# Optimization experiments

Measured on AMD Instinct MI355X. Metric: run time of the kernel, lower is better.

The kernel has to match this reference:

```python
import jax, jax.numpy as jnp
import numpy as np

B, S, E = 4, 1024, 1024
H, DH = 16, 64
P = 64  # prompt length
MASKED_BIAS = -10000.0


def setup_inputs() -> dict:
    key = jax.random.key(0)
    ks = jax.random.split(key, 9)
    return {
        "hidden_states": jax.random.normal(ks[0], (B, S, E), jnp.float32),
        "promptKey": jax.random.normal(ks[1], (B, H, P, DH), jnp.float32),
        "promptValue": jax.random.normal(ks[2], (B, H, P, DH), jnp.float32),
        "textualKey": jax.random.normal(ks[3], (B, H, S, DH), jnp.float32),
        "textualValue": jax.random.normal(ks[4], (B, H, S, DH), jnp.float32),
        "promptMask": jnp.ones((B, 1, S, P), jnp.bool_),
        "c_attn_w": jax.random.normal(ks[5], (E, 3 * E), jnp.float32) * 0.02,
        "c_attn_b": jnp.zeros((3 * E,), jnp.float32),
        "c_proj_w": jax.random.normal(ks[6], (E, E), jnp.float32) * 0.02,
        "c_proj_b": jnp.zeros((E,), jnp.float32),
    }


def _split_heads(t):
    # [B, S, E] -> [B, H, S, DH]
    b, s, _ = t.shape
    return t.reshape(b, s, H, DH).transpose(0, 2, 1, 3)


def reference(hidden_states, promptKey, promptValue, textualKey, textualValue,
              promptMask, c_attn_w, c_attn_b, c_proj_w, c_proj_b):
    qkv = hidden_states @ c_attn_w + c_attn_b          # [B,S,3E]
    q, k, v = jnp.split(qkv, 3, axis=-1)
    q, k, v = _split_heads(q), _split_heads(k), _split_heads(v)  # [B,H,S,DH]

    # scores against prompt KV, textual KV, and elementwise self term
    promptW = jnp.einsum("bhsd,bhpd->bhsp", q, promptKey)       # [B,H,S,P]
    textW = jnp.einsum("bhsd,bhtd->bhst", q, textualKey)        # [B,H,S,S]
    selfW = jnp.sum(q * k, axis=-1, keepdims=True)              # [B,H,S,1]
    attn_weights = jnp.concatenate((promptW, textW, selfW), axis=-1)
    attn_weights = attn_weights / jnp.sqrt(jnp.float32(DH))

    # non-residual causal mask: bias[qlen-qlen:qlen, 1:klen+1] -> strictly lower tri
    causal = jnp.tri(S, S, -1, dtype=bool)                      # [S,S]
    self_mask = jnp.ones((S, 1), dtype=bool)
    causal_self = jnp.concatenate((causal, self_mask), axis=-1)[None, None]  # [1,1,S,S+1]
    full_mask = jnp.concatenate(
        (promptMask, jnp.broadcast_to(causal_self, (B, 1, S, S + 1))), axis=-1)
    attn_weights = jnp.where(full_mask, attn_weights, MASKED_BIAS)
    attn_weights = jax.nn.softmax(attn_weights, axis=-1)

    wSelf = attn_weights[..., -1:]                              # [B,H,S,1]
    wRest = attn_weights[..., :-1]                              # [B,H,S,P+S]
    valuePast = jnp.concatenate((promptValue, textualValue), axis=-2)  # [B,H,P+S,DH]
    attn_output = jnp.einsum("bhsk,bhkd->bhsd", wRest, valuePast) + wSelf * v

    # merge heads and output projection
    attn_output = attn_output.transpose(0, 2, 1, 3).reshape(B, S, E)
    return attn_output @ c_proj_w + c_proj_b
```

## Files before the change

### kernel.cpp

```cpp
#include <hip/hip_runtime.h>
#include <hip/hip_bf16.h>
#include <stdint.h>

#define H_ 16
#define DH_ 64
#define S_ 1024
#define B_ 4
#define E_ 1024
#define P_ 64
#define BH_ (B_ * H_)
#define KV_ (P_ + S_)
#define NT_ 17
#define TILE_ELEMS 4096

typedef __attribute__((ext_vector_type(8))) short short8;
typedef __attribute__((ext_vector_type(4))) float floatx4;

#define MFMA_BF16(a, b, c) __builtin_amdgcn_mfma_f32_16x16x32_bf16((a), (b), (c), 0, 0, 0)

__device__ __forceinline__ float bf2f(unsigned short u) {
    union { float f; uint32_t i; } x;
    x.i = ((uint32_t)u) << 16;
    return x.f;
}
__device__ __forceinline__ unsigned short f2bf(float f) {
    uint32_t i = __float_as_uint(f);
    uint32_t r = (i + 0x7fffu + ((i >> 16) & 1u)) >> 16;
    return (unsigned short)r;
}

__device__ __forceinline__ void gl_lds16(const void* g, void* l) {
    __builtin_amdgcn_global_load_lds(
        (const __attribute__((address_space(1))) uint32_t*)g,
        (__attribute__((address_space(3))) uint32_t*)l, 16, 0, 0);
}

#define BARRIER() asm volatile("s_barrier" ::: "memory")
#define WAIT_VM(n) asm volatile("s_waitcnt vmcnt(" #n ")" ::: "memory")

__global__ void prep(const float* __restrict__ hidden, const float* __restrict__ cw,
                     const float* __restrict__ pw, const float* __restrict__ pK,
                     const float* __restrict__ tK, const float* __restrict__ pV,
                     const float* __restrict__ tV, unsigned short* __restrict__ Ah,
                     unsigned short* __restrict__ Wt1, unsigned short* __restrict__ Wt2,
                     unsigned short* __restrict__ Kp, unsigned short* __restrict__ Vp) {
    __shared__ float t[32][33];
    int bid = blockIdx.x, tid = threadIdx.x;
    if (bid < 4096) {
        int i = bid * 256 + tid;
        float4 v = ((const float4*)hidden)[i];
        ushort4 o;
        o.x = f2bf(v.x); o.y = f2bf(v.y); o.z = f2bf(v.z); o.w = f2bf(v.w);
        ((ushort4*)Ah)[i] = o;
    } else if (bid < 8192) {
        const float* in; unsigned short* out; int R, C, bxx, byy;
        if (bid < 7168) { int i = bid - 4096; in = cw; out = Wt1; R = 1024; C = 3072; bxx = i % 96; byy = i / 96; }
        else            { int i = bid - 7168; in = pw; out = Wt2; R = 1024; C = 1024; bxx = i % 32; byy = i / 32; }
        int tx = tid & 31, ty = tid >> 5;
        int c0 = bxx * 32, r0 = byy * 32;
#pragma unroll
        for (int i = 0; i < 4; ++i)
            t[ty + i * 8][tx] = in[(size_t)(r0 + ty + i * 8) * C + c0 + tx];
        __syncthreads();
#pragma unroll
        for (int i = 0; i < 4; ++i)
            out[(size_t)(c0 + ty + i * 8) * R + r0 + tx] = f2bf(t[tx][ty + i * 8]);
    } else {
        int gid0 = (bid - 8192) * 256 + tid;
        int half = gid0 / (BH_ * 8704);
        int gid = gid0 % (BH_ * 8704);
        int bh = gid / 8704, rem = gid % 8704;
        int tt = rem / 512, r2 = rem % 512;
        int f = r2 >> 6, lane = r2 & 63;
        int nt = f >> 1, h = f & 1, quad = lane >> 4, cl = lane & 15;
        unsigned short o[8];
        if (half == 0) {
            int key = tt * 64 + nt * 16 + cl;
            int dh = h * 32 + quad * 8;
            const float* src = (key < P_)
                ? pK + ((size_t)bh * P_ + key) * DH_ + dh
                : tK + ((size_t)bh * S_ + (key - P_)) * DH_ + dh;
#pragma unroll
            for (int u = 0; u < 8; ++u) o[u] = f2bf(src[u]);
            *(int4*)&Kp[(size_t)gid * 8] = *(int4*)o;
        } else {
            int dhn = nt * 16 + cl;
            int kbase = tt * 64 + h * 32 + quad * 8;
            const float* src = (kbase < P_)
                ? pV + ((size_t)bh * P_ + kbase) * DH_ + dhn
                : tV + ((size_t)bh * S_ + (kbase - P_)) * DH_ + dhn;
#pragma unroll
            for (int u = 0; u < 8; ++u) o[u] = f2bf(src[(size_t)u * DH_]);
            *(int4*)&Vp[(size_t)gid * 8] = *(int4*)o;
        }
    }
}

template <int MODE, int TM, int TN, int BK>
__global__ __launch_bounds__(256) void gemm_bt(
    const unsigned short* __restrict__ A, const unsigned short* __restrict__ Bt,
    const float* __restrict__ bias, float* __restrict__ Cout,
    unsigned short* __restrict__ Qo, unsigned short* __restrict__ Ko,
    unsigned short* __restrict__ Vo, int M, int N, int K) {
    constexpr int MI = TM / 32, NI = TN / 32;
    constexpr int NA = TM * BK / 2048;
    constexpr int NB = TN * BK / 2048;
    static_assert(NA + NB == 4, "vmcnt constant assumes 4 loads/tile");
    __shared__ __align__(16) unsigned short lA[2][TM * BK];
    __shared__ __align__(16) unsigned short lB[2][TN * BK];
    int tid = threadIdx.x;
    int wave = tid >> 6, lane = tid & 63, quad = lane >> 4, cl = lane & 15;
    int m0 = blockIdx.y * TM, n0 = blockIdx.x * TN;
    int wm = (wave >> 1) * (TM / 2), wn = (wave & 1) * (TN / 2);
    floatx4 acc[MI][NI];
#pragma unroll
    for (int mi = 0; mi < MI; ++mi)
#pragma unroll
        for (int ni = 0; ni < NI; ++ni) acc[mi][ni] = (floatx4){0.f, 0.f, 0.f, 0.f};

    auto issue = [&](int k0, int buf) {
#pragma unroll
        for (int li = 0; li < NA; ++li) {
            int o = (li * 256 + tid) * 16;
            int hh = o / (TM * 64), rr = (o % (TM * 64)) >> 6, c8 = (o >> 4) & 3;
            gl_lds16(A + (size_t)(m0 + rr) * K + k0 + hh * 32 + c8 * 8,
                     (char*)lA[buf] + o);
        }
#pragma unroll
        for (int li = 0; li < NB; ++li) {
            int o = (li * 256 + tid) * 16;
            int hh = o / (TN * 64), rr = (o % (TN * 64)) >> 6, c8 = (o >> 4) & 3;
            gl_lds16(Bt + (size_t)(n0 + rr) * K + k0 + hh * 32 + c8 * 8,
                     (char*)lB[buf] + o);
        }
    };
    auto compute = [&](int buf) {
#pragma unroll
        for (int kk = 0; kk < BK / 32; ++kk) {
            short8 af[MI], bfr[NI];
#pragma unroll
            for (int mi = 0; mi < MI; ++mi)
                af[mi] = *(const short8*)&lA[buf][kk * TM * 32 + (wm + mi * 16 + cl) * 32 + quad * 8];
#pragma unroll
            for (int ni = 0; ni < NI; ++ni)
                bfr[ni] = *(const short8*)&lB[buf][kk * TN * 32 + (wn + ni * 16 + cl) * 32 + quad * 8];
#pragma unroll
            for (int mi = 0; mi < MI; ++mi)
#pragma unroll
                for (int ni = 0; ni < NI; ++ni)
                    acc[mi][ni] = MFMA_BF16(af[mi], bfr[ni], acc[mi][ni]);
        }
    };

    int nT = K / BK;
    issue(0, 0);
    for (int t = 0; t < nT; ++t) {
        int buf = t & 1;
        if (t + 1 < nT) {
            issue((t + 1) * BK, buf ^ 1);
            WAIT_VM(4);
        } else {
            WAIT_VM(0);
        }
        BARRIER();
        compute(buf);
        BARRIER();
    }

#pragma unroll
    for (int ni = 0; ni < NI; ++ni) {
        int ncol = n0 + wn + ni * 16 + cl;
        float bv = bias[ncol];
#pragma unroll
        for (int mi = 0; mi < MI; ++mi) {
#pragma unroll
            for (int r = 0; r < 4; ++r) {
                int mrow = m0 + wm + mi * 16 + quad * 4 + r;
                float v = acc[mi][ni][r] + bv;
                if (MODE == 0) {
                    Cout[(size_t)mrow * N + ncol] = v;
                } else {
                    int which = ncol >> 10, e = ncol & 1023;
                    int hh = e >> 6, dh = e & 63;
                    int b = mrow >> 10, s = mrow & 1023;
                    size_t idx = ((size_t)(b * H_ + hh) * S_ + s) * DH_ + dh;
                    unsigned short* dst = (which == 0) ? Qo : ((which == 1) ? Ko : Vo);
                    dst[idx] = f2bf(v);
                }
            }
        }
    }
}

__global__ __launch_bounds__(256) void attn_k(
    const unsigned short* __restrict__ Q, const unsigned short* __restrict__ Kc,
    const unsigned short* __restrict__ Vc, const unsigned short* __restrict__ Kp,
    const unsigned short* __restrict__ Vp, unsigned short* __restrict__ Aout) {
    __shared__ __align__(16) unsigned short lP[4][16 * 72];
    int tid = threadIdx.x, wave = tid >> 6, lane = tid & 63;
    int quad = lane >> 4, cl = lane & 15;
    int l = blockIdx.x;
    int p = l >> 6, bh = l & 63;
    int b = bh >> 4, h = bh & 15;
    const unsigned short* Qb = Q + (size_t)bh * S_ * DH_;
    const unsigned short* Kb = Kc + (size_t)bh * S_ * DH_;
    const unsigned short* Vb = Vc + (size_t)bh * S_ * DH_;
    const unsigned short* Kpb = Kp + (size_t)bh * NT_ * TILE_ELEMS;
    const unsigned short* Vpb = Vp + (size_t)bh * NT_ * TILE_ELEMS;
    unsigned short* lp = lP[wave];

    int x1 = p, x2 = 15 - p;
    int qb1 = x1 * 64 + wave * 16, qb2 = x2 * 64 + wave * 16;

    short8 a0_1 = *(const short8*)(Qb + (size_t)(qb1 + cl) * DH_ + quad * 8);
    short8 a1_1 = *(const short8*)(Qb + (size_t)(qb1 + cl) * DH_ + quad * 8 + 32);
    short8 a0_2 = *(const short8*)(Qb + (size_t)(qb2 + cl) * DH_ + quad * 8);
    short8 a1_2 = *(const short8*)(Qb + (size_t)(qb2 + cl) * DH_ + quad * 8 + 32);

    float lsum1[4] = {0.f, 0.f, 0.f, 0.f}, lsum2[4] = {0.f, 0.f, 0.f, 0.f};
    floatx4 O1[4], O2[4];
#pragma unroll
    for (int nt = 0; nt < 4; ++nt) {
        O1[nt] = (floatx4){0.f, 0.f, 0.f, 0.f};
        O2[nt] = (floatx4){0.f, 0.f, 0.f, 0.f};
    }

    int rl = wave * 16 + quad * 4;

    auto do_tile = [&](const unsigned short* Kt, const unsigned short* Vt,
                       short8 a0, short8 a1, floatx4* O, float* lsum, bool diag) {
        floatx4 s[4];
        short8 k0[4], k1[4], v0[4], v1[4];
#pragma unroll
        for (int nt = 0; nt < 4; ++nt) {
            k0[nt] = *(const short8*)&Kt[(nt * 2 + 0) * 512 + lane * 8];
            k1[nt] = *(const short8*)&Kt[(nt * 2 + 1) * 512 + lane * 8];
        }
#pragma unroll
        for (int nt = 0; nt < 4; ++nt) {
            s[nt] = (floatx4){0.f, 0.f, 0.f, 0.f};
            s[nt] = MFMA_BF16(a0, k0[nt], s[nt]);
            s[nt] = MFMA_BF16(a1, k1[nt], s[nt]);
        }
#pragma unroll
        for (int nt = 0; nt < 4; ++nt) {
            v0[nt] = *(const short8*)&Vt[(nt * 2 + 0) * 512 + lane * 8];
            v1[nt] = *(const short8*)&Vt[(nt * 2 + 1) * 512 + lane * 8];
        }
#pragma unroll
        for (int nt = 0; nt < 4; ++nt) {
            int col = nt * 16 + cl;
#pragma unroll
            for (int r = 0; r < 4; ++r) {
                float v = s[nt][r] * 0.125f;
                if (diag && col >= rl + r) v = -10000.0f;
                float pb = __expf(v);
                lsum[r] += pb;
                lp[(quad * 4 + r) * 72 + col] = f2bf(pb);
            }
        }
        asm volatile("s_waitcnt lgkmcnt(0)" ::: "memory");
        short8 p0 = *(const short8*)&lp[cl * 72 + quad * 8];
        short8 p1 = *(const short8*)&lp[cl * 72 + quad * 8 + 32];
#pragma unroll
        for (int nt = 0; nt < 4; ++nt) {
            O[nt] = MFMA_BF16(p0, v0[nt], O[nt]);
            O[nt] = MFMA_BF16(p1, v1[nt], O[nt]);
        }
    };

    int T1 = x1 + 2, Tu = x2 + 2;
    for (int t = 0; t < Tu; ++t) {
        const unsigned short* Kt = Kpb + (size_t)t * TILE_ELEMS;
        const unsigned short* Vt = Vpb + (size_t)t * TILE_ELEMS;
        do_tile(Kt, Vt, a0_2, a1_2, O2, lsum2, t == Tu - 1);
        if (t < T1) do_tile(Kt, Vt, a0_1, a1_1, O1, lsum1, t == T1 - 1);
    }

#pragma unroll
    for (int seg = 0; seg < 2; ++seg) {
        int qb = seg ? qb2 : qb1;
        float* lsum = seg ? lsum2 : lsum1;
        floatx4* O = seg ? O2 : O1;
#pragma unroll
        for (int r = 0; r < 4; ++r) {
            float rs = lsum[r];
            rs += __shfl_xor(rs, 1, 16);
            rs += __shfl_xor(rs, 2, 16);
            rs += __shfl_xor(rs, 4, 16);
            rs += __shfl_xor(rs, 8, 16);
            int row = qb + quad * 4 + r;
            const unsigned short* qp = Qb + (size_t)row * DH_ + cl * 4;
            const unsigned short* kp = Kb + (size_t)row * DH_ + cl * 4;
            float d = 0.f;
#pragma unroll
            for (int u = 0; u < 4; ++u) d += bf2f(qp[u]) * bf2f(kp[u]);
            d += __shfl_xor(d, 1, 16);
            d += __shfl_xor(d, 2, 16);
            d += __shfl_xor(d, 4, 16);
            d += __shfl_xor(d, 8, 16);
            float ps = __expf(d * 0.125f);
            float linv = 1.0f / (rs + ps);
#pragma unroll
            for (int nt = 0; nt < 4; ++nt) {
                float vv = bf2f(Vb[(size_t)row * DH_ + nt * 16 + cl]);
                float o = (O[nt][r] + ps * vv) * linv;
                Aout[((size_t)b * S_ + row) * E_ + h * DH_ + nt * 16 + cl] = f2bf(o);
            }
        }
    }
}

extern "C" void kernel_launch(void* const* d_in, const int* in_sizes, int n_in,
                              void* d_out, int out_size, void* d_ws, size_t ws_size,
                              hipStream_t stream) {
    const float* hidden = (const float*)d_in[0];
    const float* pK = (const float*)d_in[1];
    const float* pV = (const float*)d_in[2];
    const float* tK = (const float*)d_in[3];
    const float* tV = (const float*)d_in[4];
    const float* cw = (const float*)d_in[6];
    const float* cb = (const float*)d_in[7];
    const float* pw = (const float*)d_in[8];
    const float* pb = (const float*)d_in[9];
    float* out = (float*)d_out;

    unsigned short* ws = (unsigned short*)d_ws;
    unsigned short* Wt1 = ws;
    unsigned short* Wt2 = Wt1 + (size_t)3072 * 1024;
    unsigned short* Ah  = Wt2 + (size_t)1024 * 1024;
    unsigned short* Qw  = Ah + (size_t)4096 * 1024;
    unsigned short* Kw  = Qw + (size_t)BH_ * S_ * DH_;
    unsigned short* Vw  = Kw + (size_t)BH_ * S_ * DH_;
    unsigned short* Kp  = Vw + (size_t)BH_ * S_ * DH_;
    unsigned short* Vp  = Kp + (size_t)BH_ * NT_ * TILE_ELEMS;
    unsigned short* At  = Ah;

    prep<<<12544, 256, 0, stream>>>(hidden, cw, pw, pK, tK, pV, tV,
                                    Ah, Wt1, Wt2, Kp, Vp);
    gemm_bt<1, 128, 128, 32><<<dim3(3072 / 128, 4096 / 128), 256, 0, stream>>>(
        Ah, Wt1, cb, nullptr, Qw, Kw, Vw, 4096, 3072, 1024);
    attn_k<<<512, 256, 0, stream>>>(Qw, Kw, Vw, Kp, Vp, At);
    gemm_bt<0, 64, 64, 64><<<dim3(1024 / 64, 4096 / 128 * 2), 256, 0, stream>>>(
        At, Wt2, pb, out, nullptr, nullptr, nullptr, 4096, 1024, 1024);
}
```

Before: 200.9 us.

## Add direct-B-load QKV GEMM and split attention into one tile per block

Adds a new QKV projection GEMM that stages only A through LDS with double-buffered async loads and reads the B operand directly from global memory into registers, removing the LDS traffic for B. The attention kernel no longer pairs a short and a long causal query block per workgroup. Each block now handles one 64-row query block, the grid doubles to 1024, and blocks are ordered longest-first for load balance. This trades the explicit balancing of paired work and shared K/V tile loads for more parallelism and fewer live registers per block.

```diff
diff --git a/kernel.cpp b/kernel.cpp
--- a/kernel.cpp
+++ b/kernel.cpp
@@ -192,6 +192,102 @@
     }
 }
 
+__global__ __launch_bounds__(256) void gemm_bd(
+    const unsigned short* __restrict__ A, const unsigned short* __restrict__ Bt,
+    const float* __restrict__ bias, unsigned short* __restrict__ Qo,
+    unsigned short* __restrict__ Ko, unsigned short* __restrict__ Vo,
+    int M, int N, int K) {
+    __shared__ __align__(16) unsigned short lA[2][128 * 32];
+    int tid = threadIdx.x;
+    int wave = tid >> 6, lane = tid & 63, quad = lane >> 4, cl = lane & 15;
+    int m0 = blockIdx.y * 128, n0 = blockIdx.x * 128;
+    int wm = (wave >> 1) * 64, wn = (wave & 1) * 64;
+    floatx4 acc[4][4];
+#pragma unroll
+    for (int mi = 0; mi < 4; ++mi)
+#pragma unroll
+        for (int ni = 0; ni < 4; ++ni) acc[mi][ni] = (floatx4){0.f, 0.f, 0.f, 0.f};
+
+    auto issueA = [&](int k0, int buf) {
+#pragma unroll
+        for (int li = 0; li < 2; ++li) {
+            int o = (li * 256 + tid) * 16;
+            int rr = o >> 6, c8 = (o >> 4) & 3;
+            gl_lds16(A + (size_t)(m0 + rr) * K + k0 + c8 * 8,
+                     (char*)lA[buf] + o);
+        }
+    };
+    const unsigned short* Bbase = Bt + (size_t)(n0 + wn + cl) * K + quad * 8;
+    auto loadB = [&](int k0, short8* dst) {
+#pragma unroll
+        for (int ni = 0; ni < 4; ++ni)
+            dst[ni] = *(const short8*)(Bbase + (size_t)(ni * 16) * K + k0);
+    };
+    auto compute = [&](int buf, const short8* bfr) {
+        short8 af[4];
+#pragma unroll
+        for (int mi = 0; mi < 4; ++mi)
+            af[mi] = *(const short8*)&lA[buf][(wm + mi * 16 + cl) * 32 + quad * 8];
+#pragma unroll
+        for (int mi = 0; mi < 4; ++mi)
+#pragma unroll
+            for (int ni = 0; ni < 4; ++ni)
+                acc[mi][ni] = MFMA_BF16(af[mi], bfr[ni], acc[mi][ni]);
+    };
+
+    int nT = K / 32;
+    short8 bA[4], bB[4];
+    issueA(0, 0);
+    loadB(0, bA);
+    for (int t2 = 0; t2 < nT; t2 += 2) {
+        {
+            int t = t2, buf = t & 1;
+            if (t + 1 < nT) {
+                issueA((t + 1) * 32, buf ^ 1);
+                loadB((t + 1) * 32, bB);
+                WAIT_VM(6);
+            } else {
+                WAIT_VM(0);
+            }
+            BARRIER();
+            compute(buf, bA);
+            BARRIER();
+        }
+        {
+            int t = t2 + 1, buf = t & 1;
+            if (t + 1 < nT) {
+                issueA((t + 1) * 32, buf ^ 1);
+                loadB((t + 1) * 32, bA);
+                WAIT_VM(6);
+            } else {
+                WAIT_VM(0);
+            }
+            BARRIER();
+            compute(buf, bB);
+            BARRIER();
+        }
+    }
+
+#pragma unroll
+    for (int ni = 0; ni < 4; ++ni) {
+        int ncol = n0 + wn + ni * 16 + cl;
+        float bv = bias[ncol];
+        int which = ncol >> 10, e = ncol & 1023;
+        int hh = e >> 6, dh = e & 63;
+        unsigned short* dst = (which == 0) ? Qo : ((which == 1) ? Ko : Vo);
+#pragma unroll
+        for (int mi = 0; mi < 4; ++mi) {
+#pragma unroll
+            for (int r = 0; r < 4; ++r) {
+                int mrow = m0 + wm + mi * 16 + quad * 4 + r;
+                int b = mrow >> 10, s = mrow & 1023;
+                dst[((size_t)(b * H_ + hh) * S_ + s) * DH_ + dh] =
+                    f2bf(acc[mi][ni][r] + bv);
+            }
+        }
+    }
+}
+
 __global__ __launch_bounds__(256) void attn_k(
     const unsigned short* __restrict__ Q, const unsigned short* __restrict__ Kc,
     const unsigned short* __restrict__ Vc, const unsigned short* __restrict__ Kp,
@@ -200,7 +296,7 @@
     int tid = threadIdx.x, wave = tid >> 6, lane = tid & 63;
     int quad = lane >> 4, cl = lane & 15;
     int l = blockIdx.x;
-    int p = l >> 6, bh = l & 63;
+    int x = 15 - (l >> 6), bh = l & 63;
     int b = bh >> 4, h = bh & 15;
     const unsigned short* Qb = Q + (size_t)bh * S_ * DH_;
     const unsigned short* Kb = Kc + (size_t)bh * S_ * DH_;
@@ -209,26 +305,22 @@
     const unsigned short* Vpb = Vp + (size_t)bh * NT_ * TILE_ELEMS;
     unsigned short* lp = lP[wave];
 
-    int x1 = p, x2 = 15 - p;
-    int qb1 = x1 * 64 + wave * 16, qb2 = x2 * 64 + wave * 16;
-
-    short8 a0_1 = *(const short8*)(Qb + (size_t)(qb1 + cl) * DH_ + quad * 8);
-    short8 a1_1 = *(const short8*)(Qb + (size_t)(qb1 + cl) * DH_ + quad * 8 + 32);
-    short8 a0_2 = *(const short8*)(Qb + (size_t)(qb2 + cl) * DH_ + quad * 8);
-    short8 a1_2 = *(const short8*)(Qb + (size_t)(qb2 + cl) * DH_ + quad * 8 + 32);
-
-    float lsum1[4] = {0.f, 0.f, 0.f, 0.f}, lsum2[4] = {0.f, 0.f, 0.f, 0.f};
-    floatx4 O1[4], O2[4];
-#pragma unroll
-    for (int nt = 0; nt < 4; ++nt) {
-        O1[nt] = (floatx4){0.f, 0.f, 0.f, 0.f};
-        O2[nt] = (floatx4){0.f, 0.f, 0.f, 0.f};
-    }
+    int qb = x * 64 + wave * 16;
+
+    short8 a0 = *(const short8*)(Qb + (size_t)(qb + cl) * DH_ + quad * 8);
+    short8 a1 = *(const short8*)(Qb + (size_t)(qb + cl) * DH_ + quad * 8 + 32);
+
+    float lsum[4] = {0.f, 0.f, 0.f, 0.f};
+    floatx4 O[4];
+#pragma unroll
+    for (int nt = 0; nt < 4; ++nt) O[nt] = (floatx4){0.f, 0.f, 0.f, 0.f};
 
     int rl = wave * 16 + quad * 4;
 
-    auto do_tile = [&](const unsigned short* Kt, const unsigned short* Vt,
-                       short8 a0, short8 a1, floatx4* O, float* lsum, bool diag) {
+    int T = x + 2;
+    for (int t = 0; t < T; ++t) {
+        const unsigned short* Kt = Kpb + (size_t)t * TILE_ELEMS;
+        const unsigned short* Vt = Vpb + (size_t)t * TILE_ELEMS;
         floatx4 s[4];
         short8 k0[4], k1[4], v0[4], v1[4];
 #pragma unroll
@@ -247,6 +339,7 @@
             v0[nt] = *(const short8*)&Vt[(nt * 2 + 0) * 512 + lane * 8];
             v1[nt] = *(const short8*)&Vt[(nt * 2 + 1) * 512 + lane * 8];
         }
+        bool diag = (t == T - 1);
 #pragma unroll
         for (int nt = 0; nt < 4; ++nt) {
             int col = nt * 16 + cl;
@@ -267,46 +360,32 @@
             O[nt] = MFMA_BF16(p0, v0[nt], O[nt]);
             O[nt] = MFMA_BF16(p1, v1[nt], O[nt]);
         }
-    };
-
-    int T1 = x1 + 2, Tu = x2 + 2;
-    for (int t = 0; t < Tu; ++t) {
-        const unsigned short* Kt = Kpb + (size_t)t * TILE_ELEMS;
-        const unsigned short* Vt = Vpb + (size_t)t * TILE_ELEMS;
-        do_tile(Kt, Vt, a0_2, a1_2, O2, lsum2, t == Tu - 1);
-        if (t < T1) do_tile(Kt, Vt, a0_1, a1_1, O1, lsum1, t == T1 - 1);
-    }
-
-#pragma unroll
-    for (int seg = 0; seg < 2; ++seg) {
-        int qb = seg ? qb2 : qb1;
-        float* lsum = seg ? lsum2 : lsum1;
-        floatx4* O = seg ? O2 : O1;
-#pragma unroll
-        for (int r = 0; r < 4; ++r) {
-            float rs = lsum[r];
-            rs += __shfl_xor(rs, 1, 16);
-            rs += __shfl_xor(rs, 2, 16);
-            rs += __shfl_xor(rs, 4, 16);
-            rs += __shfl_xor(rs, 8, 16);
-            int row = qb + quad * 4 + r;
-            const unsigned short* qp = Qb + (size_t)row * DH_ + cl * 4;
-            const unsigned short* kp = Kb + (size_t)row * DH_ + cl * 4;
-            float d = 0.f;
-#pragma unroll
-            for (int u = 0; u < 4; ++u) d += bf2f(qp[u]) * bf2f(kp[u]);
-            d += __shfl_xor(d, 1, 16);
-            d += __shfl_xor(d, 2, 16);
-            d += __shfl_xor(d, 4, 16);
-            d += __shfl_xor(d, 8, 16);
-            float ps = __expf(d * 0.125f);
-            float linv = 1.0f / (rs + ps);
-#pragma unroll
-            for (int nt = 0; nt < 4; ++nt) {
-                float vv = bf2f(Vb[(size_t)row * DH_ + nt * 16 + cl]);
-                float o = (O[nt][r] + ps * vv) * linv;
-                Aout[((size_t)b * S_ + row) * E_ + h * DH_ + nt * 16 + cl] = f2bf(o);
-            }
+    }
+
+#pragma unroll
+    for (int r = 0; r < 4; ++r) {
+        float rs = lsum[r];
+        rs += __shfl_xor(rs, 1, 16);
+        rs += __shfl_xor(rs, 2, 16);
+        rs += __shfl_xor(rs, 4, 16);
+        rs += __shfl_xor(rs, 8, 16);
+        int row = qb + quad * 4 + r;
+        const unsigned short* qp = Qb + (size_t)row * DH_ + cl * 4;
+        const unsigned short* kp = Kb + (size_t)row * DH_ + cl * 4;
+        float d = 0.f;
+#pragma unroll
+        for (int u = 0; u < 4; ++u) d += bf2f(qp[u]) * bf2f(kp[u]);
+        d += __shfl_xor(d, 1, 16);
+        d += __shfl_xor(d, 2, 16);
+        d += __shfl_xor(d, 4, 16);
+        d += __shfl_xor(d, 8, 16);
+        float ps = __expf(d * 0.125f);
+        float linv = 1.0f / (rs + ps);
+#pragma unroll
+        for (int nt = 0; nt < 4; ++nt) {
+            float vv = bf2f(Vb[(size_t)row * DH_ + nt * 16 + cl]);
+            float o = (O[nt][r] + ps * vv) * linv;
+            Aout[((size_t)b * S_ + row) * E_ + h * DH_ + nt * 16 + cl] = f2bf(o);
         }
     }
 }
@@ -338,9 +417,9 @@
 
     prep<<<12544, 256, 0, stream>>>(hidden, cw, pw, pK, tK, pV, tV,
                                     Ah, Wt1, Wt2, Kp, Vp);
-    gemm_bt<1, 128, 128, 32><<<dim3(3072 / 128, 4096 / 128), 256, 0, stream>>>(
-        Ah, Wt1, cb, nullptr, Qw, Kw, Vw, 4096, 3072, 1024);
-    attn_k<<<512, 256, 0, stream>>>(Qw, Kw, Vw, Kp, Vp, At);
+    gemm_bd<<<dim3(3072 / 128, 4096 / 128), 256, 0, stream>>>(
+        Ah, Wt1, cb, Qw, Kw, Vw, 4096, 3072, 1024);
+    attn_k<<<1024, 256, 0, stream>>>(Qw, Kw, Vw, Kp, Vp, At);
     gemm_bt<0, 64, 64, 64><<<dim3(1024 / 64, 4096 / 128 * 2), 256, 0, stream>>>(
         At, Wt2, pb, out, nullptr, nullptr, nullptr, 4096, 1024, 1024);
 }
```

Result: slower. 223.1 us (+11.0%).
